# Kernel optimization log

Measured on AMD Instinct MI355X. Metric: run time of the kernel, lower is better.

## Reference

```python
import jax, jax.numpy as jnp
import numpy as np

B, T, DM, H, DH = 4, 2048, 1024, 16, 64
DI = H * DH
CLIP = 1.0
LN_EPS = 1e-5


def setup_inputs() -> dict:
    key = jax.random.key(0)
    ks = jax.random.split(key, 9)

    def xav(k, shape):  # xavier_uniform, fan_in=shape[1], fan_out=shape[0]
        lim = float(np.sqrt(6.0 / (shape[0] + shape[1])))
        return jax.random.uniform(k, shape, jnp.float32, -lim, lim)

    def kai(k, shape):  # default nn.Linear weight init
        lim = float(1.0 / np.sqrt(shape[1]))
        return jax.random.uniform(k, shape, jnp.float32, -lim, lim)

    return {
        "x": jax.random.normal(ks[0], (B, T, DM), jnp.float32),
        "Wq": xav(ks[1], (DI, DM)),
        "Wk": xav(ks[2], (DI, DM)),
        "Wv": xav(ks[3], (DI, DM)),
        "Wa": kai(ks[4], (DI, DM)), "ba": jnp.full((DI,), 3.0, jnp.float32),
        "Wb": kai(ks[5], (H, DM)), "bb": jnp.zeros((H,), jnp.float32),
        "Wg": kai(ks[6], (H, DM)), "bg": jnp.zeros((H,), jnp.float32),
        "WaR": kai(ks[7], (DI, DM)), "baR": jnp.full((DI,), 3.0, jnp.float32),
        "Wo": xav(ks[8], (DM, DI)),
        "ln_w": jnp.ones((DM,), jnp.float32),
        "ln_b": jnp.zeros((DM,), jnp.float32),
    }


def reference(x, Wq, Wk, Wv, Wa, ba, Wb, bb, Wg, bg, WaR, baR, Wo, ln_w, ln_b):
    Bs, Ts, _ = x.shape
    residual = x
    # LayerNorm
    mu = jnp.mean(x, -1, keepdims=True)
    var = jnp.mean((x - mu) ** 2, -1, keepdims=True)
    xn = (x - mu) / jnp.sqrt(var + LN_EPS) * ln_w + ln_b

    q = (xn @ Wq.T).reshape(Bs, Ts, H, DH)
    k = (xn @ Wk.T).reshape(Bs, Ts, H, DH)
    v = (xn @ Wv.T).reshape(Bs, Ts, H, DH)
    alpha = jax.nn.sigmoid(xn @ Wa.T + ba).reshape(Bs, Ts, H, DH)
    aR = jax.nn.sigmoid(xn @ WaR.T + baR).reshape(Bs, Ts, H, DH)
    beta = jax.nn.sigmoid(xn @ Wb.T + bb)   # (B,T,H)
    gamma = jax.nn.sigmoid(xn @ Wg.T + bg)  # (B,T,H)

    tm = lambda a: jnp.moveaxis(a, 1, 0)  # time-major for scan
    xs = (tm(q), tm(k), tm(v), tm(alpha), tm(aR), tm(beta), tm(gamma))
    S0 = jnp.zeros((Bs, H, DH, DH), x.dtype)

    def step(carry, inp):
        S, R = carry
        q_t, k_t, v_t, a_t, aR_t, b_t, g_t = inp  # (B,H,d) / (B,H)
        kn = k_t / jnp.maximum(jnp.linalg.norm(k_t, axis=-1, keepdims=True), 1e-12)
        # residual target from previous state: r = clip(v - S^T k)
        pred = jnp.einsum('bhji,bhj->bhi', S, kn)
        r = jnp.clip(v_t - pred, -CLIP, CLIP)
        # primary state: S = diag(alpha) S; S += beta k (v - k^T S)
        S = a_t[..., None] * S
        kp = jnp.einsum('bhd,bhde->bhe', kn, S)
        S = S + b_t[..., None, None] * kn[..., None] * (v_t - kp)[..., None, :]
        o = jnp.einsum('bhji,bhj->bhi', S, q_t)
        # residual state
        R = aR_t[..., None] * R
        kpR = jnp.einsum('bhd,bhde->bhe', kn, R)
        R = R + g_t[..., None, None] * kn[..., None] * (r - kpR)[..., None, :]
        o = o + jnp.einsum('bhji,bhj->bhi', R, q_t)
        return (S, R), o

    _, os = jax.lax.scan(step, (S0, S0), xs)  # os: (T,B,H,d)
    out = jnp.moveaxis(os, 0, 1).reshape(Bs, Ts, DI) @ Wo.T
    return out + residual  # dropout is identity at inference
```

## Files before the change

kernel.cpp:

```cpp
#include <hip/hip_runtime.h>
#include <hip/hip_fp16.h>

#define B_SZ 4
#define T_SEQ 2048
#define NH 16
#define HD 64
#define DMODEL 1024
#define MTOT (B_SZ * T_SEQ)

typedef __bf16 bf16x8 __attribute__((ext_vector_type(8)));
typedef float f32x4 __attribute__((ext_vector_type(4)));
typedef float f32x2 __attribute__((ext_vector_type(2)));
typedef _Float16 f16x4 __attribute__((ext_vector_type(4)));

__device__ __forceinline__ unsigned short f2bf(float f) {
    union { float f; unsigned int i; } c; c.f = f;
    unsigned int u = c.i;
    u += 0x7fffu + ((u >> 16) & 1u);
    return (unsigned short)(u >> 16);
}
__device__ __forceinline__ float sigm(float x) { return 1.f / (1.f + __expf(-x)); }

__device__ __forceinline__ void dma16(const void* g, void* l) {
    __builtin_amdgcn_global_load_lds(
        (const __attribute__((address_space(1))) void*)g,
        (__attribute__((address_space(3))) void*)l, 16, 0, 0);
}

template <int CTRL>
__device__ __forceinline__ float dppadd(float x) {
    int v = __builtin_amdgcn_update_dpp(0, __builtin_bit_cast(int, x), CTRL, 0xf, 0xf, false);
    return x + __builtin_bit_cast(float, v);
}
__device__ __forceinline__ float rowsum16(float x) {
    x = dppadd<0x128>(x);
    x = dppadd<0x124>(x);
    x = dppadd<0x122>(x);
    x = dppadd<0x121>(x);
    return x;
}

__global__ __launch_bounds__(256, 1) void k_ln(const float* __restrict__ x,
                                               const float* __restrict__ lnw,
                                               const float* __restrict__ lnb,
                                               unsigned short* __restrict__ xn) {
    const int m = blockIdx.x;
    const int t = threadIdx.x;
    float4 xv = ((const float4*)(x + (size_t)m * DMODEL))[t];
    float s = xv.x + xv.y + xv.z + xv.w;
    float s2 = xv.x * xv.x + xv.y * xv.y + xv.z * xv.z + xv.w * xv.w;
#pragma unroll
    for (int off = 32; off >= 1; off >>= 1) {
        s += __shfl_xor(s, off);
        s2 += __shfl_xor(s2, off);
    }
    __shared__ float red[8];
    const int wid = t >> 6;
    if ((t & 63) == 0) { red[wid] = s; red[4 + wid] = s2; }
    __syncthreads();
    if (t == 0) {
        float su = red[0] + red[1] + red[2] + red[3];
        float sq = red[4] + red[5] + red[6] + red[7];
        float mu = su * (1.f / DMODEL);
        float var = sq * (1.f / DMODEL) - mu * mu;
        red[0] = mu;
        red[1] = rsqrtf(var + 1e-5f);
    }
    __syncthreads();
    float mu = red[0], rstd = red[1];
    float4 w4 = ((const float4*)lnw)[t];
    float4 b4 = ((const float4*)lnb)[t];
    ushort4 o;
    o.x = f2bf((xv.x - mu) * rstd * w4.x + b4.x);
    o.y = f2bf((xv.y - mu) * rstd * w4.y + b4.y);
    o.z = f2bf((xv.z - mu) * rstd * w4.z + b4.z);
    o.w = f2bf((xv.w - mu) * rstd * w4.w + b4.w);
    ((ushort4*)(xn + (size_t)m * DMODEL))[t] = o;
}

struct WPtrs { const float* p0; const float* p1; const float* p2; const float* p3; const float* p4; };

__global__ __launch_bounds__(256, 1) void k_wconv(WPtrs w, unsigned short* __restrict__ dst) {
    const int plane = blockIdx.y;
    const float* src = plane == 0 ? w.p0 : plane == 1 ? w.p1 : plane == 2 ? w.p2
                                                             : plane == 3 ? w.p3 : w.p4;
    const size_t i = ((size_t)blockIdx.x * 256 + threadIdx.x) * 8;
    float4 f0 = *(const float4*)(src + i);
    float4 f1 = *(const float4*)(src + i + 4);
    uint4 o;
    o.x = (unsigned)f2bf(f0.x) | ((unsigned)f2bf(f0.y) << 16);
    o.y = (unsigned)f2bf(f0.z) | ((unsigned)f2bf(f0.w) << 16);
    o.z = (unsigned)f2bf(f1.x) | ((unsigned)f2bf(f1.y) << 16);
    o.w = (unsigned)f2bf(f1.z) | ((unsigned)f2bf(f1.w) << 16);
    *(uint4*)(dst + (size_t)plane * 1048576 + i) = o;
}

__global__ __launch_bounds__(256, 1) void k_cvt1(const float* __restrict__ src,
                                                 unsigned short* __restrict__ dst) {
    const size_t i = ((size_t)blockIdx.x * 256 + threadIdx.x) * 8;
    float4 f0 = *(const float4*)(src + i);
    float4 f1 = *(const float4*)(src + i + 4);
    uint4 o;
    o.x = (unsigned)f2bf(f0.x) | ((unsigned)f2bf(f0.y) << 16);
    o.y = (unsigned)f2bf(f0.z) | ((unsigned)f2bf(f0.w) << 16);
    o.z = (unsigned)f2bf(f1.x) | ((unsigned)f2bf(f1.y) << 16);
    o.w = (unsigned)f2bf(f1.z) | ((unsigned)f2bf(f1.w) << 16);
    *(uint4*)(dst + i) = o;
}

template <int KDIM>
__device__ __forceinline__ void gemm128(const unsigned short* __restrict__ A,
                                        const unsigned short* __restrict__ Bw,
                                        int m0, int n0, f32x4 acc[4][4]) {
    __shared__ __align__(16) unsigned short sA[128 * 32];
    __shared__ __align__(16) unsigned short sB[128 * 32];

    const int t = threadIdx.x;
    const int lane = t & 63;
    const int wv = t >> 6;
    const int wm = wv >> 1, wn = wv & 1;
    const int ml = lane & 15, kq = lane >> 4;

#pragma unroll
    for (int i = 0; i < 4; i++)
#pragma unroll
        for (int j = 0; j < 4; j++) {
            f32x4 z; z[0] = 0.f; z[1] = 0.f; z[2] = 0.f; z[3] = 0.f;
            acc[i][j] = z;
        }

    const unsigned short* pA = A + (size_t)m0 * KDIM;
    const unsigned short* pB = Bw + (size_t)n0 * KDIM;
    const unsigned short* gA0 = pA + (size_t)(t >> 2) * KDIM + (t & 3) * 8;
    const unsigned short* gA1 = gA0 + (size_t)64 * KDIM;
    const unsigned short* gB0 = pB + (size_t)(t >> 2) * KDIM + (t & 3) * 8;
    const unsigned short* gB1 = gB0 + (size_t)64 * KDIM;
    unsigned short* lA0 = sA + wv * 512;
    unsigned short* lA1 = lA0 + 2048;
    unsigned short* lB0 = sB + wv * 512;
    unsigned short* lB1 = lB0 + 2048;

    for (int kb = 0; kb < KDIM / 32; kb++) {
        const int ko = kb * 32;
        dma16(gA0 + ko, lA0);
        dma16(gA1 + ko, lA1);
        dma16(gB0 + ko, lB0);
        dma16(gB1 + ko, lB1);
        __syncthreads();
        bf16x8 af[4], bfr[4];
#pragma unroll
        for (int mt = 0; mt < 4; mt++)
            af[mt] = *(const bf16x8*)&sA[(wm * 64 + mt * 16 + ml) * 32 + kq * 8];
#pragma unroll
        for (int nt = 0; nt < 4; nt++)
            bfr[nt] = *(const bf16x8*)&sB[(wn * 64 + nt * 16 + ml) * 32 + kq * 8];
#pragma unroll
        for (int mt = 0; mt < 4; mt++)
#pragma unroll
            for (int nt = 0; nt < 4; nt++)
                acc[mt][nt] = __builtin_amdgcn_mfma_f32_16x16x32_bf16(af[mt], bfr[nt], acc[mt][nt], 0, 0, 0);
        __syncthreads();
    }
}

__global__ __launch_bounds__(256, 1) void k_proj(const unsigned short* __restrict__ xn,
                                                 const unsigned short* __restrict__ wbf,
                                                 const float* __restrict__ ba,
                                                 const float* __restrict__ baR,
                                                 __half* __restrict__ qo, __half* __restrict__ ko,
                                                 __half* __restrict__ vo, __half* __restrict__ ao,
                                                 __half* __restrict__ aRo) {
    const int m0 = blockIdx.x * 128;
    const int yt = blockIdx.y;
    const int widx = yt >> 3;
    const int n0 = (yt & 7) * 128;
    const unsigned short* W = wbf + (size_t)widx * 1048576;
    f32x4 acc[4][4];
    gemm128<1024>(xn, W, m0, n0, acc);

    __half* outp = widx == 0 ? qo : widx == 1 ? ko : widx == 2 ? vo : widx == 3 ? ao : aRo;
    const float* bias = (widx == 3) ? ba : (widx == 4) ? baR : (const float*)0;
    const int lane = threadIdx.x & 63;
    const int wv = threadIdx.x >> 6;
    const int wm = wv >> 1, wn = wv & 1;
    const int ml = lane & 15, kq = lane >> 4;
#pragma unroll
    for (int mt = 0; mt < 4; mt++)
#pragma unroll
        for (int nt = 0; nt < 4; nt++) {
            const int rowg = m0 + wm * 64 + mt * 16 + kq * 4;
            const int colg = n0 + wn * 64 + nt * 16 + ml;
            float bval = bias ? bias[colg] : 0.f;
#pragma unroll
            for (int r = 0; r < 4; r++) {
                float v = acc[mt][nt][r];
                if (widx >= 3) v = sigm(v + bval);
                outp[(size_t)(rowg + r) * DMODEL + colg] = __float2half(v);
            }
        }
}

__global__ __launch_bounds__(256, 1) void k_bg(const unsigned short* __restrict__ xn,
                                               const float* __restrict__ Wb,
                                               const float* __restrict__ bb,
                                               const float* __restrict__ Wg,
                                               const float* __restrict__ bgp,
                                               f32x2* __restrict__ bgpk) {
    const int m = blockIdx.x;
    const int t = threadIdx.x;
    const int h = t >> 4, seg = t & 15;
    const ushort4* xr = (const ushort4*)(xn + (size_t)m * DMODEL + seg * 64);
    const float4* wbr = (const float4*)(Wb + (size_t)h * DMODEL + seg * 64);
    const float4* wgr = (const float4*)(Wg + (size_t)h * DMODEL + seg * 64);
    float db = 0.f, dg = 0.f;
#pragma unroll
    for (int u = 0; u < 16; u++) {
        ushort4 a = xr[u];
        float4 w1 = wbr[u], w2 = wgr[u];
        union { unsigned int i; float f; } c0, c1, c2, c3;
        c0.i = ((unsigned int)a.x) << 16; c1.i = ((unsigned int)a.y) << 16;
        c2.i = ((unsigned int)a.z) << 16; c3.i = ((unsigned int)a.w) << 16;
        db += c0.f * w1.x + c1.f * w1.y + c2.f * w1.z + c3.f * w1.w;
        dg += c0.f * w2.x + c1.f * w2.y + c2.f * w2.z + c3.f * w2.w;
    }
#pragma unroll
    for (int off = 1; off < 16; off <<= 1) {
        db += __shfl_xor(db, off);
        dg += __shfl_xor(dg, off);
    }
    if (seg == 0) {
        f32x2 o;
        o[0] = sigm(db + bb[h]);
        o[1] = sigm(dg + bgp[h]);
        bgpk[(size_t)m * NH + h] = o;
    }
}

__global__ __launch_bounds__(256, 1) void k_prep(__half* __restrict__ kb) {
    const int row = blockIdx.x * 16 + (threadIdx.x >> 4);
    const int tr = threadIdx.x & 15;
    const int bh = row >> 11, t = row & 2047;
    const size_t idx = ((size_t)((bh >> 4) * T_SEQ + t)) * DMODEL + (bh & 15) * 64 + tr * 4;
    f16x4 k4 = *(const f16x4*)((const __half*)kb + idx);
    float k0 = (float)k4[0], k1 = (float)k4[1], k2 = (float)k4[2], k3 = (float)k4[3];
    float ss = k0 * k0 + k1 * k1 + k2 * k2 + k3 * k3;
    ss = rowsum16(ss);
    float inv = 1.f / fmaxf(sqrtf(ss), 1e-12f);
    f16x4 o;
    o[0] = (_Float16)(k0 * inv); o[1] = (_Float16)(k1 * inv);
    o[2] = (_Float16)(k2 * inv); o[3] = (_Float16)(k3 * inv);
    *(f16x4*)(kb + idx) = o;
}

__global__ __launch_bounds__(256, 1) void k_scan(const __half* __restrict__ qb,
                                                 const __half* __restrict__ knb,
                                                 const __half* __restrict__ vb,
                                                 const __half* __restrict__ ab,
                                                 const __half* __restrict__ aRb,
                                                 const f32x2* __restrict__ bgpk,
                                                 unsigned short* __restrict__ ob) {
    const int blk = blockIdx.x;
    const int bh = blk & 63, cg = blk >> 6;
    const int b = bh >> 4, h = bh & 15;
    const int t = threadIdx.x;
    const int col = t >> 4, tr = t & 15;
    const int ii = cg * 16 + col;
    const int j0 = tr * 4;

    const size_t vecbase = ((size_t)b * T_SEQ) * DMODEL + h * 64 + j0;
    const size_t vbase = ((size_t)b * T_SEQ) * DMODEL + h * 64 + ii;
    const size_t bgbase = ((size_t)b * T_SEQ) * NH + h;

    const __half* pk = knb + vecbase;
    const __half* pq = qb + vecbase;
    const __half* pa = ab + vecbase;
    const __half* pr = aRb + vecbase;

    float S0 = 0, S1 = 0, S2 = 0, S3 = 0, R0 = 0, R1 = 0, R2 = 0, R3 = 0;

    f16x4 rk[6], rq[6], ra[6], rr[6];
    __half rv[6];
    f32x2 rbg[6];
    f32x4 fkn[6], fq[6], fa[6], fr[6];
    float fv[6];

#pragma unroll
    for (int p = 0; p < 6; p++) {
        const size_t voff = (size_t)p * DMODEL;
        rk[p] = *(const f16x4*)(pk + voff);
        rq[p] = *(const f16x4*)(pq + voff);
        ra[p] = *(const f16x4*)(pa + voff);
        rr[p] = *(const f16x4*)(pr + voff);
        rv[p] = vb[vbase + voff];
        rbg[p] = bgpk[bgbase + (size_t)p * NH];
    }
    fkn[0][0] = (float)rk[0][0]; fkn[0][1] = (float)rk[0][1]; fkn[0][2] = (float)rk[0][2]; fkn[0][3] = (float)rk[0][3];
    fq[0][0] = (float)rq[0][0]; fq[0][1] = (float)rq[0][1]; fq[0][2] = (float)rq[0][2]; fq[0][3] = (float)rq[0][3];
    fa[0][0] = (float)ra[0][0]; fa[0][1] = (float)ra[0][1]; fa[0][2] = (float)ra[0][2]; fa[0][3] = (float)ra[0][3];
    fr[0][0] = (float)rr[0][0]; fr[0][1] = (float)rr[0][1]; fr[0][2] = (float)rr[0][2]; fr[0][3] = (float)rr[0][3];
    fv[0] = (float)rv[0];

#define SCAN_BODY(P, PN)                                                              \
    {                                                                                 \
        const int s = st + (P);                                                       \
        const float beta = rbg[P][0], gamma = rbg[P][1];                              \
                     \
        {                                                                             \
            const size_t voff = (size_t)((s + 6) & (T_SEQ - 1)) * DMODEL;             \
            rk[P] = *(const f16x4*)(pk + voff);                                       \
            rq[P] = *(const f16x4*)(pq + voff);                                       \
            ra[P] = *(const f16x4*)(pa + voff);                                       \
            rr[P] = *(const f16x4*)(pr + voff);                                       \
            rv[P] = vb[vbase + voff];                                                 \
        }                                                                             \
                                    \
        fkn[PN][0] = (float)rk[PN][0]; fkn[PN][1] = (float)rk[PN][1];                 \
        fkn[PN][2] = (float)rk[PN][2]; fkn[PN][3] = (float)rk[PN][3];                 \
        fq[PN][0] = (float)rq[PN][0]; fq[PN][1] = (float)rq[PN][1];                   \
        fq[PN][2] = (float)rq[PN][2]; fq[PN][3] = (float)rq[PN][3];                   \
        fa[PN][0] = (float)ra[PN][0]; fa[PN][1] = (float)ra[PN][1];                   \
        fa[PN][2] = (float)ra[PN][2]; fa[PN][3] = (float)ra[PN][3];                   \
        fr[PN][0] = (float)rr[PN][0]; fr[PN][1] = (float)rr[PN][1];                   \
        fr[PN][2] = (float)rr[PN][2]; fr[PN][3] = (float)rr[PN][3];                   \
        fv[PN] = (float)rv[PN];                                                       \
                                          \
        {                                                                             \
            const float kn0 = fkn[P][0], kn1 = fkn[P][1], kn2 = fkn[P][2], kn3 = fkn[P][3]; \
            const float a0 = fa[P][0], a1 = fa[P][1], a2 = fa[P][2], a3 = fa[P][3];   \
            const float x0 = fr[P][0], x1 = fr[P][1], x2 = fr[P][2], x3 = fr[P][3];   \
            const float vc = fv[P];                                                   \
            float pred = S0 * kn0 + S1 * kn1 + S2 * kn2 + S3 * kn3;                   \
            float Sd0 = a0 * S0, Sd1 = a1 * S1, Sd2 = a2 * S2, Sd3 = a3 * S3;         \
            float Rd0 = x0 * R0, Rd1 = x1 * R1, Rd2 = x2 * R2, Rd3 = x3 * R3;         \
            float kp = Sd0 * kn0 + Sd1 * kn1 + Sd2 * kn2 + Sd3 * kn3;                 \
            float kpR = Rd0 * kn0 + Rd1 * kn1 + Rd2 * kn2 + Rd3 * kn3;                \
            pred = rowsum16(pred);                                                    \
            kp = rowsum16(kp);                                                        \
            kpR = rowsum16(kpR);                                                      \
            const float rres = fminf(fmaxf(vc - pred, -1.f), 1.f);                    \
            const float cS = beta * (vc - kp);                                        \
            const float cR = gamma * (rres - kpR);                                    \
            S0 = fmaf(cS, kn0, Sd0); S1 = fmaf(cS, kn1, Sd1);                         \
            S2 = fmaf(cS, kn2, Sd2); S3 = fmaf(cS, kn3, Sd3);                         \
            R0 = fmaf(cR, kn0, Rd0); R1 = fmaf(cR, kn1, Rd1);                         \
            R2 = fmaf(cR, kn2, Rd2); R3 = fmaf(cR, kn3, Rd3);                         \
            float o = (S0 + R0) * fq[P][0] + (S1 + R1) * fq[P][1] +                   \
                      (S2 + R2) * fq[P][2] + (S3 + R3) * fq[P][3];                    \
            o = rowsum16(o);                                                          \
            if (tr == 0 && s < T_SEQ)                                                 \
                ob[vbase + (size_t)s * DMODEL] = f2bf(o);                             \
        }                                                                             \
             \
        rbg[P] = bgpk[bgbase + (size_t)((s + 6) & (T_SEQ - 1)) * NH];                 \
    }

    for (int st = 0; st < T_SEQ; st += 6) {
        SCAN_BODY(0, 1)
        SCAN_BODY(1, 2)
        SCAN_BODY(2, 3)
        SCAN_BODY(3, 4)
        SCAN_BODY(4, 5)
        SCAN_BODY(5, 0)
    }
#undef SCAN_BODY
}

__global__ __launch_bounds__(256, 1) void k_out(const unsigned short* __restrict__ ob,
                                                const unsigned short* __restrict__ wobf,
                                                const float* __restrict__ x,
                                                float* __restrict__ out) {
    const int m0 = blockIdx.x * 128;
    const int n0 = blockIdx.y * 128;
    f32x4 acc[4][4];
    gemm128<1024>(ob, wobf, m0, n0, acc);
    const int lane = threadIdx.x & 63;
    const int wv = threadIdx.x >> 6;
    const int wm = wv >> 1, wn = wv & 1;
    const int ml = lane & 15, kq = lane >> 4;
#pragma unroll
    for (int mt = 0; mt < 4; mt++)
#pragma unroll
        for (int nt = 0; nt < 4; nt++) {
            const int rowg = m0 + wm * 64 + mt * 16 + kq * 4;
            const int colg = n0 + wn * 64 + nt * 16 + ml;
#pragma unroll
            for (int r = 0; r < 4; r++) {
                size_t idx = (size_t)(rowg + r) * DMODEL + colg;
                out[idx] = acc[mt][nt][r] + x[idx];
            }
        }
}

extern "C" void kernel_launch(void* const* d_in, const int* in_sizes, int n_in,
                              void* d_out, int out_size, void* d_ws, size_t ws_size,
                              hipStream_t stream) {
    const float* x = (const float*)d_in[0];
    const float* Wq = (const float*)d_in[1];
    const float* Wk = (const float*)d_in[2];
    const float* Wv = (const float*)d_in[3];
    const float* Wa = (const float*)d_in[4];
    const float* ba = (const float*)d_in[5];
    const float* Wb = (const float*)d_in[6];
    const float* bb = (const float*)d_in[7];
    const float* Wg = (const float*)d_in[8];
    const float* bg = (const float*)d_in[9];
    const float* WaR = (const float*)d_in[10];
    const float* baR = (const float*)d_in[11];
    const float* Wo = (const float*)d_in[12];
    const float* lnw = (const float*)d_in[13];
    const float* lnb = (const float*)d_in[14];

    const size_t SZ = 16777216ULL;
    size_t need = 6 * SZ + 2 * 1048576ULL;
    if (ws_size < need) return;

    char* ws = (char*)d_ws;
    __half* qb = (__half*)(ws + 0 * SZ);
    __half* kb = (__half*)(ws + 1 * SZ);
    __half* vb = (__half*)(ws + 2 * SZ);
    __half* ab = (__half*)(ws + 3 * SZ);
    __half* aRb = (__half*)(ws + 4 * SZ);
    unsigned short* xn = (unsigned short*)(ws + 5 * SZ);
    f32x2* bgpk = (f32x2*)(ws + 6 * SZ);

    unsigned short* wbf = (unsigned short*)d_out;
    unsigned short* wobf = (unsigned short*)qb;

    WPtrs wp{Wq, Wk, Wv, Wa, WaR};
    k_wconv<<<dim3(512, 5), dim3(256), 0, stream>>>(wp, wbf);
    k_ln<<<dim3(MTOT), dim3(256), 0, stream>>>(x, lnw, lnb, xn);
    k_proj<<<dim3(64, 40), dim3(256), 0, stream>>>(xn, wbf, ba, baR, qb, kb, vb, ab, aRb);
    k_bg<<<dim3(MTOT), dim3(256), 0, stream>>>(xn, Wb, bb, Wg, bg, bgpk);
    k_prep<<<dim3(MTOT * NH / 16), dim3(256), 0, stream>>>(kb);
    k_scan<<<dim3(256), dim3(256), 0, stream>>>(qb, kb, vb, ab, aRb, bgpk, xn);
    k_cvt1<<<dim3(512), dim3(256), 0, stream>>>(Wo, wobf);
    k_out<<<dim3(64, 8), dim3(256), 0, stream>>>(xn, wobf, x, (float*)d_out);
}
```

Measured before the change: 944.4 us.

## Add fp32 intermediate path for scan with packed-math recurrence and batched row sums

When the workspace is large enough, projections are written as fp32 instead of fp16, and a new fp32 scan kernel uses packed two-wide float math. It also batches the output row-sum reductions over three timesteps, taking them off the per-step critical path. This removes the fp16-to-fp32 conversions in the serial scan loop. In exchange it doubles the memory traffic for the projection outputs and the scan loads, and it needs a larger workspace.

```diff
diff --git a/kernel.cpp b/kernel.cpp
--- a/kernel.cpp
+++ b/kernel.cpp
@@ -38,6 +38,12 @@
     x = dppadd<0x122>(x);
     x = dppadd<0x121>(x);
     return x;
+}
+
+__device__ __forceinline__ void rowsum3(float& a, float& b, float& c) {
+    a = rowsum16(a);
+    b = rowsum16(b);
+    c = rowsum16(c);
 }
 
 __global__ __launch_bounds__(256, 1) void k_ln(const float* __restrict__ x,
@@ -163,13 +169,14 @@
     }
 }
 
+template <typename OT>
 __global__ __launch_bounds__(256, 1) void k_proj(const unsigned short* __restrict__ xn,
                                                  const unsigned short* __restrict__ wbf,
                                                  const float* __restrict__ ba,
                                                  const float* __restrict__ baR,
-                                                 __half* __restrict__ qo, __half* __restrict__ ko,
-                                                 __half* __restrict__ vo, __half* __restrict__ ao,
-                                                 __half* __restrict__ aRo) {
+                                                 OT* __restrict__ qo, OT* __restrict__ ko,
+                                                 OT* __restrict__ vo, OT* __restrict__ ao,
+                                                 OT* __restrict__ aRo) {
     const int m0 = blockIdx.x * 128;
     const int yt = blockIdx.y;
     const int widx = yt >> 3;
@@ -178,7 +185,7 @@
     f32x4 acc[4][4];
     gemm128<1024>(xn, W, m0, n0, acc);
 
-    __half* outp = widx == 0 ? qo : widx == 1 ? ko : widx == 2 ? vo : widx == 3 ? ao : aRo;
+    OT* outp = widx == 0 ? qo : widx == 1 ? ko : widx == 2 ? vo : widx == 3 ? ao : aRo;
     const float* bias = (widx == 3) ? ba : (widx == 4) ? baR : (const float*)0;
     const int lane = threadIdx.x & 63;
     const int wv = threadIdx.x >> 6;
@@ -195,7 +202,7 @@
             for (int r = 0; r < 4; r++) {
                 float v = acc[mt][nt][r];
                 if (widx >= 3) v = sigm(v + bval);
-                outp[(size_t)(rowg + r) * DMODEL + colg] = __float2half(v);
+                outp[(size_t)(rowg + r) * DMODEL + colg] = (OT)v;
             }
         }
 }
@@ -236,7 +243,7 @@
     }
 }
 
-__global__ __launch_bounds__(256, 1) void k_prep(__half* __restrict__ kb) {
+__global__ __launch_bounds__(256, 1) void k_prep16(__half* __restrict__ kb) {
     const int row = blockIdx.x * 16 + (threadIdx.x >> 4);
     const int tr = threadIdx.x & 15;
     const int bh = row >> 11, t = row & 2047;
@@ -252,13 +259,132 @@
     *(f16x4*)(kb + idx) = o;
 }
 
-__global__ __launch_bounds__(256, 1) void k_scan(const __half* __restrict__ qb,
-                                                 const __half* __restrict__ knb,
-                                                 const __half* __restrict__ vb,
-                                                 const __half* __restrict__ ab,
-                                                 const __half* __restrict__ aRb,
-                                                 const f32x2* __restrict__ bgpk,
-                                                 unsigned short* __restrict__ ob) {
+__global__ __launch_bounds__(256, 1) void k_prep32(float* __restrict__ kb) {
+    const int row = blockIdx.x * 16 + (threadIdx.x >> 4);
+    const int tr = threadIdx.x & 15;
+    const int bh = row >> 11, t = row & 2047;
+    const size_t idx = ((size_t)((bh >> 4) * T_SEQ + t)) * DMODEL + (bh & 15) * 64 + tr * 4;
+    f32x4 k4 = *(const f32x4*)(kb + idx);
+    float ss = k4[0] * k4[0] + k4[1] * k4[1] + k4[2] * k4[2] + k4[3] * k4[3];
+    ss = rowsum16(ss);
+    float inv = 1.f / fmaxf(sqrtf(ss), 1e-12f);
+    f32x4 o;
+    o[0] = k4[0] * inv; o[1] = k4[1] * inv; o[2] = k4[2] * inv; o[3] = k4[3] * inv;
+    *(f32x4*)(kb + idx) = o;
+}
+
+__global__ __launch_bounds__(256, 1) void k_scan32(const float* __restrict__ qb,
+                                                   const float* __restrict__ knb,
+                                                   const float* __restrict__ vb,
+                                                   const float* __restrict__ ab,
+                                                   const float* __restrict__ aRb,
+                                                   const f32x2* __restrict__ bgpk,
+                                                   unsigned short* __restrict__ ob) {
+    const int blk = blockIdx.x;
+    const int bh = blk & 63, cg = blk >> 6;
+    const int b = bh >> 4, h = bh & 15;
+    const int t = threadIdx.x;
+    const int col = t >> 4, tr = t & 15;
+    const int ii = cg * 16 + col;
+    const int j0 = tr * 4;
+
+    const size_t blkoff = (size_t)b * T_SEQ * DMODEL + h * 64;
+    const float* pq = qb + blkoff;
+    const float* pk = knb + blkoff;
+    const float* pa = ab + blkoff;
+    const float* pr = aRb + blkoff;
+    const float* pvb = vb + blkoff;
+    const f32x2* pbg = bgpk + (size_t)b * T_SEQ * NH + h;
+    unsigned short* obp = ob + blkoff + ii;
+
+    f32x2 S01 = {0.f, 0.f}, S23 = {0.f, 0.f}, R01 = {0.f, 0.f}, R23 = {0.f, 0.f};
+
+    f32x4 rk[6], rq[6], ra[6], rr[6];
+    float rv[6];
+    f32x2 rbg[6];
+
+#pragma unroll
+    for (int p = 0; p < 6; p++) {
+        const size_t vo = (size_t)p * DMODEL;
+        rk[p] = *(const f32x4*)(pk + vo + j0);
+        rq[p] = *(const f32x4*)(pq + vo + j0);
+        ra[p] = *(const f32x4*)(pa + vo + j0);
+        rr[p] = *(const f32x4*)(pr + vo + j0);
+        rv[p] = pvb[vo + ii];
+        rbg[p] = pbg[(size_t)p * NH];
+    }
+
+    float oA, oB, oC;
+
+#define SCAN_BODY32(P, ODEST)                                                       \
+    {                                                                               \
+        const f32x2 kn01 = {rk[P][0], rk[P][1]}, kn23 = {rk[P][2], rk[P][3]};       \
+        const f32x2 a01 = {ra[P][0], ra[P][1]}, a23 = {ra[P][2], ra[P][3]};         \
+        const f32x2 x01 = {rr[P][0], rr[P][1]}, x23 = {rr[P][2], rr[P][3]};         \
+        const f32x2 q01 = {rq[P][0], rq[P][1]}, q23 = {rq[P][2], rq[P][3]};         \
+        const float vc = rv[P];                                                     \
+        const float beta = rbg[P][0], gamma = rbg[P][1];                            \
+        const f32x2 Sd01 = a01 * S01, Sd23 = a23 * S23;                             \
+        const f32x2 Rd01 = x01 * R01, Rd23 = x23 * R23;                             \
+        const f32x2 pv2 = S01 * kn01 + S23 * kn23;                                  \
+        const f32x2 kp2 = Sd01 * kn01 + Sd23 * kn23;                                \
+        const f32x2 kR2 = Rd01 * kn01 + Rd23 * kn23;                                \
+        float pred = pv2[0] + pv2[1];                                               \
+        float kp = kp2[0] + kp2[1];                                                 \
+        float kpR = kR2[0] + kR2[1];                                                \
+        rowsum3(pred, kp, kpR);                                                     \
+        const float rres = fminf(fmaxf(vc - pred, -1.f), 1.f);                      \
+        const float cS = beta * (vc - kp);                                          \
+        const float cR = gamma * (rres - kpR);                                      \
+        const f32x2 cS2 = {cS, cS}, cR2 = {cR, cR};                                 \
+        S01 = cS2 * kn01 + Sd01; S23 = cS2 * kn23 + Sd23;                           \
+        R01 = cR2 * kn01 + Rd01; R23 = cR2 * kn23 + Rd23;                           \
+        const f32x2 ov = (S01 + R01) * q01 + (S23 + R23) * q23;                     \
+        ODEST = ov[0] + ov[1];                                                      \
+              \
+        {                                                                           \
+            const int sp = (st + (P) + 6) & (T_SEQ - 1);                            \
+            const size_t vo = (size_t)sp * DMODEL;                                  \
+            rk[P] = *(const f32x4*)(pk + vo + j0);                                  \
+            rq[P] = *(const f32x4*)(pq + vo + j0);                                  \
+            ra[P] = *(const f32x4*)(pa + vo + j0);                                  \
+            rr[P] = *(const f32x4*)(pr + vo + j0);                                  \
+            rv[P] = pvb[vo + ii];                                                   \
+            rbg[P] = pbg[(size_t)sp * NH];                                          \
+        }                                                                           \
+    }
+
+#define FLUSH3(SBASE)                                                               \
+    {                                                                               \
+        rowsum3(oA, oB, oC);                                                        \
+        if (tr == 0) {                                                              \
+            if ((SBASE) < T_SEQ)     obp[(size_t)(SBASE) * DMODEL] = f2bf(oA);      \
+            if ((SBASE) + 1 < T_SEQ) obp[(size_t)((SBASE) + 1) * DMODEL] = f2bf(oB);\
+            if ((SBASE) + 2 < T_SEQ) obp[(size_t)((SBASE) + 2) * DMODEL] = f2bf(oC);\
+        }                                                                           \
+    }
+
+    for (int st = 0; st < T_SEQ; st += 6) {
+        SCAN_BODY32(0, oA)
+        SCAN_BODY32(1, oB)
+        SCAN_BODY32(2, oC)
+        FLUSH3(st)
+        SCAN_BODY32(3, oA)
+        SCAN_BODY32(4, oB)
+        SCAN_BODY32(5, oC)
+        FLUSH3(st + 3)
+    }
+#undef SCAN_BODY32
+#undef FLUSH3
+}
+
+__global__ __launch_bounds__(256, 1) void k_scan16(const __half* __restrict__ qb,
+                                                   const __half* __restrict__ knb,
+                                                   const __half* __restrict__ vb,
+                                                   const __half* __restrict__ ab,
+                                                   const __half* __restrict__ aRb,
+                                                   const f32x2* __restrict__ bgpk,
+                                                   unsigned short* __restrict__ ob) {
     const int blk = blockIdx.x;
     const int bh = blk & 63, cg = blk >> 6;
     const int b = bh >> 4, h = bh & 15;
@@ -304,7 +430,6 @@
     {                                                                                 \
         const int s = st + (P);                                                       \
         const float beta = rbg[P][0], gamma = rbg[P][1];                              \
-                     \
         {                                                                             \
             const size_t voff = (size_t)((s + 6) & (T_SEQ - 1)) * DMODEL;             \
             rk[P] = *(const f16x4*)(pk + voff);                                       \
@@ -313,7 +438,6 @@
             rr[P] = *(const f16x4*)(pr + voff);                                       \
             rv[P] = vb[vbase + voff];                                                 \
         }                                                                             \
-                                    \
         fkn[PN][0] = (float)rk[PN][0]; fkn[PN][1] = (float)rk[PN][1];                 \
         fkn[PN][2] = (float)rk[PN][2]; fkn[PN][3] = (float)rk[PN][3];                 \
         fq[PN][0] = (float)rq[PN][0]; fq[PN][1] = (float)rq[PN][1];                   \
@@ -323,7 +447,6 @@
         fr[PN][0] = (float)rr[PN][0]; fr[PN][1] = (float)rr[PN][1];                   \
         fr[PN][2] = (float)rr[PN][2]; fr[PN][3] = (float)rr[PN][3];                   \
         fv[PN] = (float)rv[PN];                                                       \
-                                          \
         {                                                                             \
             const float kn0 = fkn[P][0], kn1 = fkn[P][1], kn2 = fkn[P][2], kn3 = fkn[P][3]; \
             const float a0 = fa[P][0], a1 = fa[P][1], a2 = fa[P][2], a3 = fa[P][3];   \
@@ -350,7 +473,6 @@
             if (tr == 0 && s < T_SEQ)                                                 \
                 ob[vbase + (size_t)s * DMODEL] = f2bf(o);                             \
         }                                                                             \
-             \
         rbg[P] = bgpk[bgbase + (size_t)((s + 6) & (T_SEQ - 1)) * NH];                 \
     }
 
@@ -410,29 +532,51 @@
     const float* lnw = (const float*)d_in[13];
     const float* lnb = (const float*)d_in[14];
 
-    const size_t SZ = 16777216ULL;
-    size_t need = 6 * SZ + 2 * 1048576ULL;
-    if (ws_size < need) return;
+    const size_t SZH = 16777216ULL;
+    const size_t SZF = 33554432ULL;
+    const size_t need32 = 5 * SZF + SZH + 2097152ULL;
+    const size_t need16 = 6 * SZH + 2097152ULL;
 
     char* ws = (char*)d_ws;
-    __half* qb = (__half*)(ws + 0 * SZ);
-    __half* kb = (__half*)(ws + 1 * SZ);
-    __half* vb = (__half*)(ws + 2 * SZ);
-    __half* ab = (__half*)(ws + 3 * SZ);
-    __half* aRb = (__half*)(ws + 4 * SZ);
-    unsigned short* xn = (unsigned short*)(ws + 5 * SZ);
-    f32x2* bgpk = (f32x2*)(ws + 6 * SZ);
-
     unsigned short* wbf = (unsigned short*)d_out;
-    unsigned short* wobf = (unsigned short*)qb;
-
     WPtrs wp{Wq, Wk, Wv, Wa, WaR};
-    k_wconv<<<dim3(512, 5), dim3(256), 0, stream>>>(wp, wbf);
-    k_ln<<<dim3(MTOT), dim3(256), 0, stream>>>(x, lnw, lnb, xn);
-    k_proj<<<dim3(64, 40), dim3(256), 0, stream>>>(xn, wbf, ba, baR, qb, kb, vb, ab, aRb);
-    k_bg<<<dim3(MTOT), dim3(256), 0, stream>>>(xn, Wb, bb, Wg, bg, bgpk);
-    k_prep<<<dim3(MTOT * NH / 16), dim3(256), 0, stream>>>(kb);
-    k_scan<<<dim3(256), dim3(256), 0, stream>>>(qb, kb, vb, ab, aRb, bgpk, xn);
-    k_cvt1<<<dim3(512), dim3(256), 0, stream>>>(Wo, wobf);
-    k_out<<<dim3(64, 8), dim3(256), 0, stream>>>(xn, wobf, x, (float*)d_out);
-}
+
+    if (ws_size >= need32) {
+        float* qb = (float*)(ws + 0 * SZF);
+        float* kb = (float*)(ws + 1 * SZF);
+        float* vb = (float*)(ws + 2 * SZF);
+        float* ab = (float*)(ws + 3 * SZF);
+        float* aRb = (float*)(ws + 4 * SZF);
+        unsigned short* xn = (unsigned short*)(ws + 5 * SZF);
+        f32x2* bgpk = (f32x2*)(ws + 5 * SZF + SZH);
+        unsigned short* wobf = (unsigned short*)qb;
+
+        k_wconv<<<dim3(512, 5), dim3(256), 0, stream>>>(wp, wbf);
+        k_ln<<<dim3(MTOT), dim3(256), 0, stream>>>(x, lnw, lnb, xn);
+        k_proj<float><<<dim3(64, 40), dim3(256), 0, stream>>>(xn, wbf, ba, baR, qb, kb, vb, ab, aRb);
+        k_bg<<<dim3(MTOT), dim3(256), 0, stream>>>(xn, Wb, bb, Wg, bg, bgpk);
+        k_prep32<<<dim3(MTOT * NH / 16), dim3(256), 0, stream>>>(kb);
+        k_scan32<<<dim3(256), dim3(256), 0, stream>>>(qb, kb, vb, ab, aRb, bgpk, xn);
+        k_cvt1<<<dim3(512), dim3(256), 0, stream>>>(Wo, wobf);
+        k_out<<<dim3(64, 8), dim3(256), 0, stream>>>(xn, wobf, x, (float*)d_out);
+    } else if (ws_size >= need16) {
+        __half* qb = (__half*)(ws + 0 * SZH);
+        __half* kb = (__half*)(ws + 1 * SZH);
+        __half* vb = (__half*)(ws + 2 * SZH);
+        __half* ab = (__half*)(ws + 3 * SZH);
+        __half* aRb = (__half*)(ws + 4 * SZH);
+        unsigned short* xn = (unsigned short*)(ws + 5 * SZH);
+        f32x2* bgpk = (f32x2*)(ws + 6 * SZH);
+        unsigned short* wobf = (unsigned short*)qb;
+
+        k_wconv<<<dim3(512, 5), dim3(256), 0, stream>>>(wp, wbf);
+        k_ln<<<dim3(MTOT), dim3(256), 0, stream>>>(x, lnw, lnb, xn);
+        k_proj<_Float16><<<dim3(64, 40), dim3(256), 0, stream>>>(
+            xn, wbf, ba, baR, (_Float16*)qb, (_Float16*)kb, (_Float16*)vb, (_Float16*)ab, (_Float16*)aRb);
+        k_bg<<<dim3(MTOT), dim3(256), 0, stream>>>(xn, Wb, bb, Wg, bg, bgpk);
+        k_prep16<<<dim3(MTOT * NH / 16), dim3(256), 0, stream>>>(kb);
+        k_scan16<<<dim3(256), dim3(256), 0, stream>>>(qb, kb, vb, ab, aRb, bgpk, xn);
+        k_cvt1<<<dim3(512), dim3(256), 0, stream>>>(Wo, wobf);
+        k_out<<<dim3(64, 8), dim3(256), 0, stream>>>(xn, wobf, x, (float*)d_out);
+    }
+}
```

New measurement: 835.5 us. 11.5% less time.
